# Kernel optimization log

Measured on AMD Instinct MI355X. Metric: run time of the kernel, lower is better.

## Reference

```python
import jax, jax.numpy as jnp
import numpy as np

N_NODES = 50000
N_EDGES = 800000
IN_CH = 256
HID = 512
NUM_LAYERS = 3
EPS = 1e-12  # F.normalize eps


def setup_inputs() -> dict:
    key = jax.random.key(0)
    ks = jax.random.split(key, 2 + 3 * NUM_LAYERS)
    x = jax.random.normal(ks[0], (N_NODES, IN_CH), dtype=jnp.float32)
    edge_index = jax.random.randint(ks[1], (2, N_EDGES), 0, N_NODES, dtype=jnp.int64)
    inp = {"x": x, "edge_index": edge_index}
    dims = [(IN_CH, HID)] + [(HID, HID)] * (NUM_LAYERS - 1)
    for i, (din, dout) in enumerate(dims):
        s = 1.0 / np.sqrt(din)
        inp[f"Wl{i}"] = jax.random.normal(ks[2 + 3 * i], (din, dout), dtype=jnp.float32) * s
        inp[f"bl{i}"] = jnp.zeros((dout,), dtype=jnp.float32)
        inp[f"Wr{i}"] = jax.random.normal(ks[3 + 3 * i], (din, dout), dtype=jnp.float32) * s
    return inp


def _sage_conv(x, src, dst, Wl, bl, Wr):
    # aggr='add': out[dst] += x[src], then lin_l(agg) + lin_r(x), L2 normalize rows
    agg = jax.ops.segment_sum(x[src], dst, num_segments=x.shape[0])  # [N, din]
    out = agg @ Wl + bl + x @ Wr  # [N, dout]
    norm = jnp.maximum(jnp.linalg.norm(out, axis=-1, keepdims=True), EPS)
    return out / norm


def reference(x, edge_index, Wl0, bl0, Wr0, Wl1, bl1, Wr1, Wl2, bl2, Wr2):
    src, dst = edge_index[0], edge_index[1]
    feat = x
    params = [(Wl0, bl0, Wr0), (Wl1, bl1, Wr1), (Wl2, bl2, Wr2)]
    for Wl, bl, Wr in params:
        aggre = _sage_conv(feat, src, dst, Wl, bl, Wr)
        # Dropout(p=0.15) is identity in eval mode
        feat = jax.nn.elu(aggre)
    return feat
```

## Files before the change

kernel.cpp:

```cpp
#include <hip/hip_runtime.h>
#include <math.h>

#define N_NODES 50000
#define M_PAD   50048
#define N_EDGES 800000
#define HID 512

typedef short bf16x8 __attribute__((ext_vector_type(8)));
typedef float f32x4  __attribute__((ext_vector_type(4)));
typedef unsigned short u16x4 __attribute__((ext_vector_type(4)));
typedef unsigned short u16x8 __attribute__((ext_vector_type(8)));

__device__ inline float b2f(unsigned short u) {
    union { unsigned int i; float f; } v; v.i = ((unsigned int)u) << 16; return v.f;
}
__device__ inline unsigned short f2b(float f) {
    union { float f; unsigned int i; } v; v.f = f;
    unsigned int r = v.i + 0x7FFFu + ((v.i >> 16) & 1u);
    return (unsigned short)(r >> 16);
}


__global__ void zero_kernel(int* __restrict__ p, int n) {
    int i = blockIdx.x * blockDim.x + threadIdx.x;
    if (i < n) p[i] = 0;
}

__global__ void detect_kernel(const int* __restrict__ e, int* __restrict__ flag) {
    if (blockIdx.x == 0 && threadIdx.x == 0) {
        int is64 = 1;
        for (int i = 0; i < 16; ++i)
            if (e[2 * i + 1] != 0) is64 = 0;
        *flag = is64;
    }
}

__global__ void hist_kernel(const void* __restrict__ eidx, const int* __restrict__ flag,
                            int* __restrict__ counts) {
    int e = blockIdx.x * blockDim.x + threadIdx.x;
    if (e >= N_EDGES) return;
    int is64 = *flag;
    int d;
    if (is64) d = (int)((const long long*)eidx)[N_EDGES + e];
    else      d = ((const int*)eidx)[N_EDGES + e];
    atomicAdd(&counts[d], 1);
}

__global__ __launch_bounds__(1024) void scan_kernel(const int* __restrict__ counts,
                                                    int* __restrict__ offsets) {
    __shared__ int sums[1024];
    int t = threadIdx.x;
    const int CH = (N_NODES + 1023) / 1024;
    int lo = t * CH;
    int hi = min(lo + CH, N_NODES);
    int s = 0;
    for (int i = lo; i < hi; ++i) s += counts[i];
    sums[t] = s;
    __syncthreads();
    for (int off = 1; off < 1024; off <<= 1) {
        int v = 0;
        if (t >= off) v = sums[t - off];
        __syncthreads();
        sums[t] += v;
        __syncthreads();
    }
    int excl = (t == 0) ? 0 : sums[t - 1];
    for (int i = lo; i < hi; ++i) { offsets[i] = excl; excl += counts[i]; }
    if (t == 1023) offsets[N_NODES] = excl;
}

__global__ void fill_kernel(const void* __restrict__ eidx, const int* __restrict__ flag,
                            const int* __restrict__ offsets, int* __restrict__ cursor,
                            int* __restrict__ edge_src) {
    int e = blockIdx.x * blockDim.x + threadIdx.x;
    if (e >= N_EDGES) return;
    int is64 = *flag;
    int s, d;
    if (is64) {
        const long long* p = (const long long*)eidx;
        s = (int)p[e];
        d = (int)p[N_EDGES + e];
    } else {
        const int* p = (const int*)eidx;
        s = p[e];
        d = p[N_EDGES + e];
    }
    int pos = atomicAdd(&cursor[d], 1);
    edge_src[offsets[d] + pos] = s;
}


__global__ __launch_bounds__(256) void xconv_kernel(const float* __restrict__ x,
                                                    unsigned short* __restrict__ cat1) {
    int id = blockIdx.x * 256 + threadIdx.x;
    if (id >= M_PAD * 64) return;
    int row = id >> 6;
    int c = (id & 63) * 4;
    float4 v = make_float4(0.f, 0.f, 0.f, 0.f);
    if (row < N_NODES) v = *(const float4*)(x + (size_t)row * 256 + c);
    ushort4 h;
    h.x = f2b(v.x); h.y = f2b(v.y); h.z = f2b(v.z); h.w = f2b(v.w);
    *(ushort4*)(cat1 + (size_t)row * 512 + 256 + c) = h;
}

__global__ __launch_bounds__(128) void wconv_kernel(const float* __restrict__ W,
                                                    unsigned short* __restrict__ T,
                                                    int K, int ktot, int off) {
    int n = blockIdx.x;
    for (int k = threadIdx.x; k < K; k += 128)
        T[(size_t)n * ktot + off + k] = f2b(W[(size_t)k * HID + n]);
}


template <int EPL>
__global__ __launch_bounds__(256) void aggregate_kernel(const unsigned short* __restrict__ Fh,
                                                        const int* __restrict__ off,
                                                        const int* __restrict__ esrc,
                                                        unsigned short* __restrict__ Ah) {
    const int STRIDE = 2 * EPL * 64;
    const int wid = threadIdx.x >> 6;
    const int lane = threadIdx.x & 63;
    const int node = blockIdx.x * 4 + wid;
    if (node >= N_NODES) return;
    const int beg = off[node], end = off[node + 1];
    const int deg = end - beg;
    const int lb = lane * EPL;
    using VecT = typename std::conditional<EPL == 8, u16x8, u16x4>::type;

    float a0[EPL], a1[EPL], a2[EPL], a3[EPL];
#pragma unroll
    for (int j = 0; j < EPL; ++j) { a0[j] = 0.f; a1[j] = 0.f; a2[j] = 0.f; a3[j] = 0.f; }

    int idxv = 0;

#define ACC(ARR, S)                                                         \
    {                                                                       \
        VecT v_ = *(const VecT*)(Fh + (size_t)(S) * STRIDE + lb);           \
        _Pragma("unroll")                                                   \
        for (int j_ = 0; j_ < EPL; ++j_) ARR[j_] += b2f(v_[j_]);            \
    }

    for (int i = 0; i < deg; i += 4) {
        const int b = i & 63;
        if (b == 0) idxv = (beg + i + lane < end) ? esrc[beg + i + lane] : 0;
        const int s0 = __shfl(idxv, b);
        const int s1 = __shfl(idxv, b + 1);
        const int s2 = __shfl(idxv, b + 2);
        const int s3 = __shfl(idxv, b + 3);
        ACC(a0, s0);
        if (i + 1 < deg) ACC(a1, s1);
        if (i + 2 < deg) ACC(a2, s2);
        if (i + 3 < deg) ACC(a3, s3);
    }
#undef ACC

    unsigned short* op = Ah + (size_t)node * STRIDE + lb;
    VecT h;
#pragma unroll
    for (int j = 0; j < EPL; ++j) h[j] = f2b(a0[j] + a1[j] + a2[j] + a3[j]);
    __builtin_nontemporal_store(h, (VecT*)op);
}


template <int FINAL>
__global__ __launch_bounds__(512, 2) void gemm_mfma_kernel(
    const unsigned short* __restrict__ A, const unsigned short* __restrict__ B,
    const float* __restrict__ bias, float* __restrict__ outF,
    unsigned short* __restrict__ pre, int K) {
    __shared__ unsigned short S[2 * 12288];
    const int T = gridDim.x;
    const int q = T >> 3, r = T & 7;
    const int xcd = blockIdx.x & 7;
    const int n0 = blockIdx.x >> 3;
    const int g = xcd * q + min(xcd, r) + n0;
    const int bm = (g >> 1) * 128;
    const int bn = (g & 1) * 256;

    const int tid = threadIdx.x;
    const int l = tid & 63;
    const int w = tid >> 6;
    const int wr = (w >> 2) * 64;
    const int wc = (w & 3) * 64;

    const int se = (tid >> 2) * 32 + (tid & 3) * 8;
    const unsigned short* gA  = A + (size_t)(bm + (tid >> 2)) * K + (tid & 3) * 8;
    const unsigned short* gB0 = B + (size_t)(bn + (tid >> 2)) * K + (tid & 3) * 8;
    const unsigned short* gB1 = B + (size_t)(bn + 128 + (tid >> 2)) * K + (tid & 3) * 8;

    f32x4 acc[4][4];
#pragma unroll
    for (int m = 0; m < 4; ++m)
#pragma unroll
        for (int nn = 0; nn < 4; ++nn) acc[m][nn] = (f32x4){0.f, 0.f, 0.f, 0.f};

    const int aoff = (wr + (l & 15)) * 32 + (l >> 4) * 8;
    const int woff = 4096 + (wc + (l & 15)) * 32 + (l >> 4) * 8;
    const int ktiles = K >> 5;

    auto STAGE = [&](int buf, int kt) {
        unsigned short* lb = &S[buf * 12288];
        __builtin_amdgcn_global_load_lds(
            (const __attribute__((address_space(1))) void*)(gA + kt * 32),
            (__attribute__((address_space(3))) void*)(lb + se), 16, 0, 0);
        __builtin_amdgcn_global_load_lds(
            (const __attribute__((address_space(1))) void*)(gB0 + kt * 32),
            (__attribute__((address_space(3))) void*)(lb + 4096 + se), 16, 0, 0);
        __builtin_amdgcn_global_load_lds(
            (const __attribute__((address_space(1))) void*)(gB1 + kt * 32),
            (__attribute__((address_space(3))) void*)(lb + 8192 + se), 16, 0, 0);
    };

    STAGE(0, 0);
    __syncthreads();

    for (int kt = 0; kt < ktiles; ++kt) {
        if (kt + 1 < ktiles) STAGE((kt + 1) & 1, kt + 1);
        const int sb = (kt & 1) * 12288;

        bf16x8 af[4], wf[4];
#pragma unroll
        for (int m = 0; m < 4; ++m)
            af[m] = *(const bf16x8*)&S[sb + aoff + m * 512];
#pragma unroll
        for (int nn = 0; nn < 4; ++nn)
            wf[nn] = *(const bf16x8*)&S[sb + woff + nn * 512];
#pragma unroll
        for (int m = 0; m < 4; ++m)
#pragma unroll
            for (int nn = 0; nn < 4; ++nn)
                acc[m][nn] = __builtin_amdgcn_mfma_f32_16x16x32_bf16(af[m], wf[nn], acc[m][nn], 0, 0, 0);
        __syncthreads();
    }

    const int r0 = bm + wr + (l >> 4) * 4;
    const int c0 = bn + wc + (l & 15);
#pragma unroll
    for (int nn = 0; nn < 4; ++nn) {
        const float bv = bias[c0 + nn * 16];
#pragma unroll
        for (int m = 0; m < 4; ++m) {
#pragma unroll
            for (int j = 0; j < 4; ++j) {
                int gr = r0 + m * 16 + j;
                if (gr < N_NODES) {
                    float val = acc[m][nn][j] + bv;
                    if constexpr (FINAL)
                        outF[(size_t)gr * HID + c0 + nn * 16] = val;
                    else
                        pre[(size_t)gr * HID + c0 + nn * 16] = f2b(val);
                }
            }
        }
    }
}


template <int FINAL>
__global__ __launch_bounds__(256) void norm_elu_kernel(const void* __restrict__ inp,
                                                       float* __restrict__ outF,
                                                       unsigned short* __restrict__ Fh) {
    const int wid = threadIdx.x >> 6;
    const int lane = threadIdx.x & 63;
    const int row = blockIdx.x * 4 + wid;
    if (row >= N_NODES) return;
    float r[8];
    if constexpr (FINAL) {
        const float* p = (const float*)inp + (size_t)row * HID + lane * 8;
        float4 v0 = *(const float4*)p;
        float4 v1 = *(const float4*)(p + 4);
        r[0] = v0.x; r[1] = v0.y; r[2] = v0.z; r[3] = v0.w;
        r[4] = v1.x; r[5] = v1.y; r[6] = v1.z; r[7] = v1.w;
    } else {
        const unsigned short* p = (const unsigned short*)inp + (size_t)row * HID + lane * 8;
        u16x8 v = *(const u16x8*)p;
#pragma unroll
        for (int j = 0; j < 8; ++j) r[j] = b2f(v[j]);
    }
    float ss = 0.f;
#pragma unroll
    for (int j = 0; j < 8; ++j) ss += r[j] * r[j];
#pragma unroll
    for (int o = 32; o > 0; o >>= 1) ss += __shfl_xor(ss, o);
    float inv = 1.f / fmaxf(sqrtf(ss), 1e-12f);
#pragma unroll
    for (int j = 0; j < 8; ++j) {
        r[j] *= inv;
        r[j] = r[j] > 0.f ? r[j] : expm1f(r[j]);
    }
    if constexpr (FINAL) {
        float* q = outF + (size_t)row * HID + lane * 8;
        *(float4*)q = make_float4(r[0], r[1], r[2], r[3]);
        *(float4*)(q + 4) = make_float4(r[4], r[5], r[6], r[7]);
    } else {
        unsigned short* q = Fh + (size_t)row * 1024 + lane * 8;
        u16x8 h;
#pragma unroll
        for (int j = 0; j < 8; ++j) h[j] = f2b(r[j]);
        *(u16x8*)q = h;
    }
}


extern "C" void kernel_launch(void* const* d_in, const int* in_sizes, int n_in,
                              void* d_out, int out_size, void* d_ws, size_t ws_size,
                              hipStream_t stream) {
    const float* x    = (const float*)d_in[0];
    const void*  eidx = d_in[1];
    const float* Wl0 = (const float*)d_in[2];
    const float* bl0 = (const float*)d_in[3];
    const float* Wr0 = (const float*)d_in[4];
    const float* Wl1 = (const float*)d_in[5];
    const float* bl1 = (const float*)d_in[6];
    const float* Wr1 = (const float*)d_in[7];
    const float* Wl2 = (const float*)d_in[8];
    const float* bl2 = (const float*)d_in[9];
    const float* Wr2 = (const float*)d_in[10];
    float* outF = (float*)d_out;
    unsigned short* preB = (unsigned short*)d_out;

    char* ws = (char*)d_ws;
    size_t o = 0;
    auto alloc = [&](size_t bytes) { void* p = ws + o; o += (bytes + 255) & ~(size_t)255; return p; };

    unsigned short* Cat1 = (unsigned short*)alloc((size_t)M_PAD * 512 * 2);
    unsigned short* Cat2 = (unsigned short*)alloc((size_t)M_PAD * 1024 * 2);

    unsigned short* Wcat0 = (unsigned short*)alloc(512 * 512 * 2);
    unsigned short* Wcat1 = (unsigned short*)alloc(512 * 1024 * 2);
    unsigned short* Wcat2 = (unsigned short*)alloc(512 * 1024 * 2);

    int* counts   = (int*)alloc((size_t)2 * N_NODES * 4);
    int* cursor   = counts + N_NODES;
    int* offsets  = (int*)alloc((size_t)(N_NODES + 1) * 4);
    int* edge_src = (int*)alloc((size_t)N_EDGES * 4);
    int* flag     = (int*)alloc(256);

    zero_kernel<<<(2 * N_NODES + 255) / 256, 256, 0, stream>>>(counts, 2 * N_NODES);
    detect_kernel<<<1, 64, 0, stream>>>((const int*)eidx, flag);
    hist_kernel<<<(N_EDGES + 255) / 256, 256, 0, stream>>>(eidx, flag, counts);
    scan_kernel<<<1, 1024, 0, stream>>>(counts, offsets);
    fill_kernel<<<(N_EDGES + 255) / 256, 256, 0, stream>>>(eidx, flag, offsets, cursor, edge_src);

    xconv_kernel<<<(M_PAD * 64 + 255) / 256, 256, 0, stream>>>(x, Cat1);
    wconv_kernel<<<512, 128, 0, stream>>>(Wl0, Wcat0, 256, 512, 0);
    wconv_kernel<<<512, 128, 0, stream>>>(Wr0, Wcat0, 256, 512, 256);
    wconv_kernel<<<512, 128, 0, stream>>>(Wl1, Wcat1, 512, 1024, 0);
    wconv_kernel<<<512, 128, 0, stream>>>(Wr1, Wcat1, 512, 1024, 512);
    wconv_kernel<<<512, 128, 0, stream>>>(Wl2, Wcat2, 512, 1024, 0);
    wconv_kernel<<<512, 128, 0, stream>>>(Wr2, Wcat2, 512, 1024, 512);

    const int ggrid = 2 * (M_PAD / 128);
    const int nchunk = (N_NODES + 3) / 4;

    aggregate_kernel<4><<<nchunk, 256, 0, stream>>>(Cat1 + 256, offsets, edge_src, Cat1);
    gemm_mfma_kernel<0><<<ggrid, 512, 0, stream>>>(Cat1, Wcat0, bl0, nullptr, preB, 512);
    norm_elu_kernel<0><<<nchunk, 256, 0, stream>>>(preB, nullptr, Cat2 + 512);

    aggregate_kernel<8><<<nchunk, 256, 0, stream>>>(Cat2 + 512, offsets, edge_src, Cat2);
    gemm_mfma_kernel<0><<<ggrid, 512, 0, stream>>>(Cat2, Wcat1, bl1, nullptr, preB, 1024);
    norm_elu_kernel<0><<<nchunk, 256, 0, stream>>>(preB, nullptr, Cat2 + 512);

    aggregate_kernel<8><<<nchunk, 256, 0, stream>>>(Cat2 + 512, offsets, edge_src, Cat2);
    gemm_mfma_kernel<1><<<ggrid, 512, 0, stream>>>(Cat2, Wcat2, bl2, outF, nullptr, 1024);
    norm_elu_kernel<1><<<nchunk, 256, 0, stream>>>(outF, outF, nullptr);

    (void)in_sizes; (void)n_in; (void)out_size; (void)ws_size;
}
```

Measured before the change: 783.3 us.

## Overlap root GEMM with neighbor aggregation in a combined heterogeneous kernel

The concatenated [agg|x]·[Wl;Wr] GEMM is split in two. The x·Wr half runs in the same launch as the gather aggregation: the first NP blocks do the MFMA GEMM and the rest aggregate 8 nodes each, so compute-bound and memory-bound work can share the GPU. A second GEMM computes agg·Wl and adds the bf16 partial product P in its epilogue. The weight conversions and the zero/detect launches are merged, which cuts launch count. The cost is an extra bf16 round trip of P through memory, extra rounding of the partial product, and a halved K per GEMM.

```diff
diff --git a/kernel.cpp b/kernel.cpp
--- a/kernel.cpp
+++ b/kernel.cpp
@@ -21,16 +21,14 @@
 }
 
 
-__global__ void zero_kernel(int* __restrict__ p, int n) {
+__global__ void zero_detect_kernel(int* __restrict__ p, int n,
+                                   const int* __restrict__ e, int* __restrict__ flag) {
     int i = blockIdx.x * blockDim.x + threadIdx.x;
     if (i < n) p[i] = 0;
-}
-
-__global__ void detect_kernel(const int* __restrict__ e, int* __restrict__ flag) {
     if (blockIdx.x == 0 && threadIdx.x == 0) {
         int is64 = 1;
-        for (int i = 0; i < 16; ++i)
-            if (e[2 * i + 1] != 0) is64 = 0;
+        for (int k = 0; k < 16; ++k)
+            if (e[2 * k + 1] != 0) is64 = 0;
         *flag = is64;
     }
 }
@@ -91,7 +89,7 @@
 
 
 __global__ __launch_bounds__(256) void xconv_kernel(const float* __restrict__ x,
-                                                    unsigned short* __restrict__ cat1) {
+                                                    unsigned short* __restrict__ feat) {
     int id = blockIdx.x * 256 + threadIdx.x;
     if (id >= M_PAD * 64) return;
     int row = id >> 6;
@@ -100,73 +98,162 @@
     if (row < N_NODES) v = *(const float4*)(x + (size_t)row * 256 + c);
     ushort4 h;
     h.x = f2b(v.x); h.y = f2b(v.y); h.z = f2b(v.z); h.w = f2b(v.w);
-    *(ushort4*)(cat1 + (size_t)row * 512 + 256 + c) = h;
-}
-
-__global__ __launch_bounds__(128) void wconv_kernel(const float* __restrict__ W,
-                                                    unsigned short* __restrict__ T,
-                                                    int K, int ktot, int off) {
+    *(ushort4*)(feat + (size_t)row * 256 + c) = h;
+}
+
+__global__ __launch_bounds__(128) void wconv_all_kernel(
+    const float* __restrict__ Wl0, const float* __restrict__ Wr0,
+    const float* __restrict__ Wl1, const float* __restrict__ Wr1,
+    const float* __restrict__ Wl2, const float* __restrict__ Wr2,
+    unsigned short* __restrict__ Tl0, unsigned short* __restrict__ Tr0,
+    unsigned short* __restrict__ Tl1, unsigned short* __restrict__ Tr1,
+    unsigned short* __restrict__ Tl2, unsigned short* __restrict__ Tr2) {
+    const int y = blockIdx.y;
+    const float* W = (y == 0) ? Wl0 : (y == 1) ? Wr0 : (y == 2) ? Wl1
+                   : (y == 3) ? Wr1 : (y == 4) ? Wl2 : Wr2;
+    unsigned short* T = (y == 0) ? Tl0 : (y == 1) ? Tr0 : (y == 2) ? Tl1
+                      : (y == 3) ? Tr1 : (y == 4) ? Tl2 : Tr2;
+    const int K = (y < 2) ? 256 : 512;
     int n = blockIdx.x;
     for (int k = threadIdx.x; k < K; k += 128)
-        T[(size_t)n * ktot + off + k] = f2b(W[(size_t)k * HID + n]);
-}
-
-
-template <int EPL>
-__global__ __launch_bounds__(256) void aggregate_kernel(const unsigned short* __restrict__ Fh,
-                                                        const int* __restrict__ off,
-                                                        const int* __restrict__ esrc,
-                                                        unsigned short* __restrict__ Ah) {
-    const int STRIDE = 2 * EPL * 64;
-    const int wid = threadIdx.x >> 6;
-    const int lane = threadIdx.x & 63;
-    const int node = blockIdx.x * 4 + wid;
-    if (node >= N_NODES) return;
-    const int beg = off[node], end = off[node + 1];
-    const int deg = end - beg;
-    const int lb = lane * EPL;
-    using VecT = typename std::conditional<EPL == 8, u16x8, u16x4>::type;
-
-    float a0[EPL], a1[EPL], a2[EPL], a3[EPL];
-#pragma unroll
-    for (int j = 0; j < EPL; ++j) { a0[j] = 0.f; a1[j] = 0.f; a2[j] = 0.f; a3[j] = 0.f; }
-
-    int idxv = 0;
-
-#define ACC(ARR, S)                                                         \
-    {                                                                       \
-        VecT v_ = *(const VecT*)(Fh + (size_t)(S) * STRIDE + lb);           \
-        _Pragma("unroll")                                                   \
-        for (int j_ = 0; j_ < EPL; ++j_) ARR[j_] += b2f(v_[j_]);            \
-    }
-
-    for (int i = 0; i < deg; i += 4) {
-        const int b = i & 63;
-        if (b == 0) idxv = (beg + i + lane < end) ? esrc[beg + i + lane] : 0;
-        const int s0 = __shfl(idxv, b);
-        const int s1 = __shfl(idxv, b + 1);
-        const int s2 = __shfl(idxv, b + 2);
-        const int s3 = __shfl(idxv, b + 3);
-        ACC(a0, s0);
-        if (i + 1 < deg) ACC(a1, s1);
-        if (i + 2 < deg) ACC(a2, s2);
-        if (i + 3 < deg) ACC(a3, s3);
-    }
+        T[(size_t)n * K + k] = f2b(W[(size_t)k * HID + n]);
+}
+
+
+template <int DIN>
+__global__ __launch_bounds__(512, 2) void fat_kernel(
+    const unsigned short* __restrict__ feat, const unsigned short* __restrict__ W2t,
+    unsigned short* __restrict__ P,
+    const int* __restrict__ off, const int* __restrict__ esrc,
+    unsigned short* __restrict__ agg, int NP) {
+    __shared__ unsigned short S[2 * 12288];
+    const int tid = threadIdx.x;
+
+    if ((int)blockIdx.x < NP) {
+        const int T = NP;
+        const int q = T >> 3, r = T & 7;
+        const int xcd = blockIdx.x & 7;
+        const int n0 = blockIdx.x >> 3;
+        const int g = xcd * q + min(xcd, r) + n0;
+        const int bm = (g >> 1) * 128;
+        const int bn = (g & 1) * 256;
+
+        const int l = tid & 63;
+        const int w = tid >> 6;
+        const int wr = (w >> 2) * 64;
+        const int wc = (w & 3) * 64;
+
+        const int se = (tid >> 2) * 32 + (tid & 3) * 8;
+        const unsigned short* gA  = feat + (size_t)(bm + (tid >> 2)) * DIN + (tid & 3) * 8;
+        const unsigned short* gB0 = W2t + (size_t)(bn + (tid >> 2)) * DIN + (tid & 3) * 8;
+        const unsigned short* gB1 = W2t + (size_t)(bn + 128 + (tid >> 2)) * DIN + (tid & 3) * 8;
+
+        f32x4 acc[4][4];
+#pragma unroll
+        for (int m = 0; m < 4; ++m)
+#pragma unroll
+            for (int nn = 0; nn < 4; ++nn) acc[m][nn] = (f32x4){0.f, 0.f, 0.f, 0.f};
+
+        const int aoff = (wr + (l & 15)) * 32 + (l >> 4) * 8;
+        const int woff = 4096 + (wc + (l & 15)) * 32 + (l >> 4) * 8;
+        const int ktiles = DIN >> 5;
+
+        auto STAGE = [&](int buf, int kt) {
+            unsigned short* lb = &S[buf * 12288];
+            __builtin_amdgcn_global_load_lds(
+                (const __attribute__((address_space(1))) void*)(gA + kt * 32),
+                (__attribute__((address_space(3))) void*)(lb + se), 16, 0, 0);
+            __builtin_amdgcn_global_load_lds(
+                (const __attribute__((address_space(1))) void*)(gB0 + kt * 32),
+                (__attribute__((address_space(3))) void*)(lb + 4096 + se), 16, 0, 0);
+            __builtin_amdgcn_global_load_lds(
+                (const __attribute__((address_space(1))) void*)(gB1 + kt * 32),
+                (__attribute__((address_space(3))) void*)(lb + 8192 + se), 16, 0, 0);
+        };
+
+        STAGE(0, 0);
+        __syncthreads();
+        for (int kt = 0; kt < ktiles; ++kt) {
+            if (kt + 1 < ktiles) STAGE((kt + 1) & 1, kt + 1);
+            const int sb = (kt & 1) * 12288;
+            bf16x8 af[4], wf[4];
+#pragma unroll
+            for (int m = 0; m < 4; ++m)
+                af[m] = *(const bf16x8*)&S[sb + aoff + m * 512];
+#pragma unroll
+            for (int nn = 0; nn < 4; ++nn)
+                wf[nn] = *(const bf16x8*)&S[sb + woff + nn * 512];
+#pragma unroll
+            for (int m = 0; m < 4; ++m)
+#pragma unroll
+                for (int nn = 0; nn < 4; ++nn)
+                    acc[m][nn] = __builtin_amdgcn_mfma_f32_16x16x32_bf16(af[m], wf[nn], acc[m][nn], 0, 0, 0);
+            __syncthreads();
+        }
+
+        const int r0 = bm + wr + (l >> 4) * 4;
+        const int c0 = bn + wc + (l & 15);
+#pragma unroll
+        for (int nn = 0; nn < 4; ++nn) {
+#pragma unroll
+            for (int m = 0; m < 4; ++m) {
+#pragma unroll
+                for (int j = 0; j < 4; ++j) {
+                    int gr = r0 + m * 16 + j;
+                    if (gr < N_NODES)
+                        P[(size_t)gr * HID + c0 + nn * 16] = f2b(acc[m][nn][j]);
+                }
+            }
+        }
+    } else {
+        const int EPL = DIN / 64;
+        const int wid = tid >> 6;
+        const int lane = tid & 63;
+        const int node = (blockIdx.x - NP) * 8 + wid;
+        if (node >= N_NODES) return;
+        const int beg = off[node], end = off[node + 1];
+        const int deg = end - beg;
+        const int lb = lane * EPL;
+        using VecT = typename std::conditional<EPL == 8, u16x8, u16x4>::type;
+
+        float a0[EPL], a1[EPL], a2[EPL], a3[EPL];
+#pragma unroll
+        for (int j = 0; j < EPL; ++j) { a0[j] = 0.f; a1[j] = 0.f; a2[j] = 0.f; a3[j] = 0.f; }
+
+        int idxv = 0;
+#define ACC(ARR, SS)                                                        \
+        {                                                                   \
+            VecT v_ = *(const VecT*)(feat + (size_t)(SS) * DIN + lb);       \
+            _Pragma("unroll")                                               \
+            for (int j_ = 0; j_ < EPL; ++j_) ARR[j_] += b2f(v_[j_]);        \
+        }
+        for (int i = 0; i < deg; i += 4) {
+            const int b = i & 63;
+            if (b == 0) idxv = (beg + i + lane < end) ? esrc[beg + i + lane] : 0;
+            const int s0 = __shfl(idxv, b);
+            const int s1 = __shfl(idxv, b + 1);
+            const int s2 = __shfl(idxv, b + 2);
+            const int s3 = __shfl(idxv, b + 3);
+            ACC(a0, s0);
+            if (i + 1 < deg) ACC(a1, s1);
+            if (i + 2 < deg) ACC(a2, s2);
+            if (i + 3 < deg) ACC(a3, s3);
+        }
 #undef ACC
-
-    unsigned short* op = Ah + (size_t)node * STRIDE + lb;
-    VecT h;
-#pragma unroll
-    for (int j = 0; j < EPL; ++j) h[j] = f2b(a0[j] + a1[j] + a2[j] + a3[j]);
-    __builtin_nontemporal_store(h, (VecT*)op);
-}
-
-
-template <int FINAL>
-__global__ __launch_bounds__(512, 2) void gemm_mfma_kernel(
+        unsigned short* op = agg + (size_t)node * DIN + lb;
+        VecT h;
+#pragma unroll
+        for (int j = 0; j < EPL; ++j) h[j] = f2b(a0[j] + a1[j] + a2[j] + a3[j]);
+        __builtin_nontemporal_store(h, (VecT*)op);
+    }
+}
+
+
+template <int FINAL, int DIN>
+__global__ __launch_bounds__(512, 2) void gemm2_kernel(
     const unsigned short* __restrict__ A, const unsigned short* __restrict__ B,
-    const float* __restrict__ bias, float* __restrict__ outF,
-    unsigned short* __restrict__ pre, int K) {
+    const unsigned short* __restrict__ P, const float* __restrict__ bias,
+    float* __restrict__ outF, unsigned short* __restrict__ pre) {
     __shared__ unsigned short S[2 * 12288];
     const int T = gridDim.x;
     const int q = T >> 3, r = T & 7;
@@ -183,9 +270,9 @@
     const int wc = (w & 3) * 64;
 
     const int se = (tid >> 2) * 32 + (tid & 3) * 8;
-    const unsigned short* gA  = A + (size_t)(bm + (tid >> 2)) * K + (tid & 3) * 8;
-    const unsigned short* gB0 = B + (size_t)(bn + (tid >> 2)) * K + (tid & 3) * 8;
-    const unsigned short* gB1 = B + (size_t)(bn + 128 + (tid >> 2)) * K + (tid & 3) * 8;
+    const unsigned short* gA  = A + (size_t)(bm + (tid >> 2)) * DIN + (tid & 3) * 8;
+    const unsigned short* gB0 = B + (size_t)(bn + (tid >> 2)) * DIN + (tid & 3) * 8;
+    const unsigned short* gB1 = B + (size_t)(bn + 128 + (tid >> 2)) * DIN + (tid & 3) * 8;
 
     f32x4 acc[4][4];
 #pragma unroll
@@ -195,7 +282,7 @@
 
     const int aoff = (wr + (l & 15)) * 32 + (l >> 4) * 8;
     const int woff = 4096 + (wc + (l & 15)) * 32 + (l >> 4) * 8;
-    const int ktiles = K >> 5;
+    const int ktiles = DIN >> 5;
 
     auto STAGE = [&](int buf, int kt) {
         unsigned short* lb = &S[buf * 12288];
@@ -212,11 +299,9 @@
 
     STAGE(0, 0);
     __syncthreads();
-
     for (int kt = 0; kt < ktiles; ++kt) {
         if (kt + 1 < ktiles) STAGE((kt + 1) & 1, kt + 1);
         const int sb = (kt & 1) * 12288;
-
         bf16x8 af[4], wf[4];
 #pragma unroll
         for (int m = 0; m < 4; ++m)
@@ -243,7 +328,8 @@
             for (int j = 0; j < 4; ++j) {
                 int gr = r0 + m * 16 + j;
                 if (gr < N_NODES) {
-                    float val = acc[m][nn][j] + bv;
+                    float val = acc[m][nn][j] + bv
+                              + b2f(P[(size_t)gr * HID + c0 + nn * 16]);
                     if constexpr (FINAL)
                         outF[(size_t)gr * HID + c0 + nn * 16] = val;
                     else
@@ -258,7 +344,7 @@
 template <int FINAL>
 __global__ __launch_bounds__(256) void norm_elu_kernel(const void* __restrict__ inp,
                                                        float* __restrict__ outF,
-                                                       unsigned short* __restrict__ Fh) {
+                                                       unsigned short* __restrict__ feat) {
     const int wid = threadIdx.x >> 6;
     const int lane = threadIdx.x & 63;
     const int row = blockIdx.x * 4 + wid;
@@ -288,15 +374,15 @@
         r[j] = r[j] > 0.f ? r[j] : expm1f(r[j]);
     }
     if constexpr (FINAL) {
-        float* q = outF + (size_t)row * HID + lane * 8;
-        *(float4*)q = make_float4(r[0], r[1], r[2], r[3]);
-        *(float4*)(q + 4) = make_float4(r[4], r[5], r[6], r[7]);
+        float* qp = outF + (size_t)row * HID + lane * 8;
+        *(float4*)qp = make_float4(r[0], r[1], r[2], r[3]);
+        *(float4*)(qp + 4) = make_float4(r[4], r[5], r[6], r[7]);
     } else {
-        unsigned short* q = Fh + (size_t)row * 1024 + lane * 8;
+        unsigned short* qp = feat + (size_t)row * HID + lane * 8;
         u16x8 h;
 #pragma unroll
         for (int j = 0; j < 8; ++j) h[j] = f2b(r[j]);
-        *(u16x8*)q = h;
+        *(u16x8*)qp = h;
     }
 }
 
@@ -322,12 +408,16 @@
     size_t o = 0;
     auto alloc = [&](size_t bytes) { void* p = ws + o; o += (bytes + 255) & ~(size_t)255; return p; };
 
-    unsigned short* Cat1 = (unsigned short*)alloc((size_t)M_PAD * 512 * 2);
-    unsigned short* Cat2 = (unsigned short*)alloc((size_t)M_PAD * 1024 * 2);
-
-    unsigned short* Wcat0 = (unsigned short*)alloc(512 * 512 * 2);
-    unsigned short* Wcat1 = (unsigned short*)alloc(512 * 1024 * 2);
-    unsigned short* Wcat2 = (unsigned short*)alloc(512 * 1024 * 2);
+    unsigned short* featB = (unsigned short*)alloc((size_t)M_PAD * 512 * 2);
+    unsigned short* aggB  = (unsigned short*)alloc((size_t)M_PAD * 512 * 2);
+    unsigned short* Pbuf  = (unsigned short*)alloc((size_t)M_PAD * 512 * 2);
+
+    unsigned short* Wl0t = (unsigned short*)alloc(512 * 256 * 2);
+    unsigned short* Wr0t = (unsigned short*)alloc(512 * 256 * 2);
+    unsigned short* Wl1t = (unsigned short*)alloc(512 * 512 * 2);
+    unsigned short* Wr1t = (unsigned short*)alloc(512 * 512 * 2);
+    unsigned short* Wl2t = (unsigned short*)alloc(512 * 512 * 2);
+    unsigned short* Wr2t = (unsigned short*)alloc(512 * 512 * 2);
 
     int* counts   = (int*)alloc((size_t)2 * N_NODES * 4);
     int* cursor   = counts + N_NODES;
@@ -335,33 +425,33 @@
     int* edge_src = (int*)alloc((size_t)N_EDGES * 4);
     int* flag     = (int*)alloc(256);
 
-    zero_kernel<<<(2 * N_NODES + 255) / 256, 256, 0, stream>>>(counts, 2 * N_NODES);
-    detect_kernel<<<1, 64, 0, stream>>>((const int*)eidx, flag);
+    zero_detect_kernel<<<(2 * N_NODES + 255) / 256, 256, 0, stream>>>(
+        counts, 2 * N_NODES, (const int*)eidx, flag);
     hist_kernel<<<(N_EDGES + 255) / 256, 256, 0, stream>>>(eidx, flag, counts);
     scan_kernel<<<1, 1024, 0, stream>>>(counts, offsets);
     fill_kernel<<<(N_EDGES + 255) / 256, 256, 0, stream>>>(eidx, flag, offsets, cursor, edge_src);
 
-    xconv_kernel<<<(M_PAD * 64 + 255) / 256, 256, 0, stream>>>(x, Cat1);
-    wconv_kernel<<<512, 128, 0, stream>>>(Wl0, Wcat0, 256, 512, 0);
-    wconv_kernel<<<512, 128, 0, stream>>>(Wr0, Wcat0, 256, 512, 256);
-    wconv_kernel<<<512, 128, 0, stream>>>(Wl1, Wcat1, 512, 1024, 0);
-    wconv_kernel<<<512, 128, 0, stream>>>(Wr1, Wcat1, 512, 1024, 512);
-    wconv_kernel<<<512, 128, 0, stream>>>(Wl2, Wcat2, 512, 1024, 0);
-    wconv_kernel<<<512, 128, 0, stream>>>(Wr2, Wcat2, 512, 1024, 512);
-
-    const int ggrid = 2 * (M_PAD / 128);
+    xconv_kernel<<<(M_PAD * 64 + 255) / 256, 256, 0, stream>>>(x, featB);
+    {
+        dim3 wgrid(512, 6);
+        wconv_all_kernel<<<wgrid, 128, 0, stream>>>(Wl0, Wr0, Wl1, Wr1, Wl2, Wr2,
+                                                    Wl0t, Wr0t, Wl1t, Wr1t, Wl2t, Wr2t);
+    }
+
+    const int NP = 2 * (M_PAD / 128);
+    const int NG = (N_NODES + 7) / 8;
     const int nchunk = (N_NODES + 3) / 4;
 
-    aggregate_kernel<4><<<nchunk, 256, 0, stream>>>(Cat1 + 256, offsets, edge_src, Cat1);
-    gemm_mfma_kernel<0><<<ggrid, 512, 0, stream>>>(Cat1, Wcat0, bl0, nullptr, preB, 512);
-    norm_elu_kernel<0><<<nchunk, 256, 0, stream>>>(preB, nullptr, Cat2 + 512);
-
-    aggregate_kernel<8><<<nchunk, 256, 0, stream>>>(Cat2 + 512, offsets, edge_src, Cat2);
-    gemm_mfma_kernel<0><<<ggrid, 512, 0, stream>>>(Cat2, Wcat1, bl1, nullptr, preB, 1024);
-    norm_elu_kernel<0><<<nchunk, 256, 0, stream>>>(preB, nullptr, Cat2 + 512);
-
-    aggregate_kernel<8><<<nchunk, 256, 0, stream>>>(Cat2 + 512, offsets, edge_src, Cat2);
-    gemm_mfma_kernel<1><<<ggrid, 512, 0, stream>>>(Cat2, Wcat2, bl2, outF, nullptr, 1024);
+    fat_kernel<256><<<NP + NG, 512, 0, stream>>>(featB, Wr0t, Pbuf, offsets, edge_src, aggB, NP);
+    gemm2_kernel<0, 256><<<NP, 512, 0, stream>>>(aggB, Wl0t, Pbuf, bl0, nullptr, preB);
+    norm_elu_kernel<0><<<nchunk, 256, 0, stream>>>(preB, nullptr, featB);
+
+    fat_kernel<512><<<NP + NG, 512, 0, stream>>>(featB, Wr1t, Pbuf, offsets, edge_src, aggB, NP);
+    gemm2_kernel<0, 512><<<NP, 512, 0, stream>>>(aggB, Wl1t, Pbuf, bl1, nullptr, preB);
+    norm_elu_kernel<0><<<nchunk, 256, 0, stream>>>(preB, nullptr, featB);
+
+    fat_kernel<512><<<NP + NG, 512, 0, stream>>>(featB, Wr2t, Pbuf, offsets, edge_src, aggB, NP);
+    gemm2_kernel<1, 512><<<NP, 512, 0, stream>>>(aggB, Wl2t, Pbuf, bl2, outF, nullptr);
     norm_elu_kernel<1><<<nchunk, 256, 0, stream>>>(outF, outF, nullptr);
 
     (void)in_sizes; (void)n_in; (void)out_size; (void)ws_size;
```

After: 1.084 ms. +38.3%, slower.

## Replace GEMM with 256x256-tile, 8-phase pipelined MFMA kernel with swizzled LDS

Applied to the files above, without the earlier changes.

Swaps the 128x256-tile double-buffered GEMM for a 256x256-tile kernel with BK=64. Each K-tile is split into half-tile phases that interleave global-to-LDS staging with MFMA work, using explicit vmcnt waits, barriers and s_setprio. It adds an XOR swizzle to the LDS layout to cut bank conflicts and pads M to a multiple of 256. The aim is more operand reuse per LDS load and better overlap of memory traffic with compute, at the cost of one block per CU (128KB LDS, more registers). The zero and detect setup kernels are also merged into one launch.

```diff
diff --git a/kernel.cpp b/kernel.cpp
--- a/kernel.cpp
+++ b/kernel.cpp
@@ -2,7 +2,7 @@
 #include <math.h>
 
 #define N_NODES 50000
-#define M_PAD   50048
+#define M_PAD   50176
 #define N_EDGES 800000
 #define HID 512
 
@@ -21,16 +21,14 @@
 }
 
 
-__global__ void zero_kernel(int* __restrict__ p, int n) {
+__global__ void zero_detect_kernel(int* __restrict__ p, int n,
+                                   const int* __restrict__ e, int* __restrict__ flag) {
     int i = blockIdx.x * blockDim.x + threadIdx.x;
     if (i < n) p[i] = 0;
-}
-
-__global__ void detect_kernel(const int* __restrict__ e, int* __restrict__ flag) {
     if (blockIdx.x == 0 && threadIdx.x == 0) {
         int is64 = 1;
-        for (int i = 0; i < 16; ++i)
-            if (e[2 * i + 1] != 0) is64 = 0;
+        for (int k = 0; k < 16; ++k)
+            if (e[2 * k + 1] != 0) is64 = 0;
         *flag = is64;
     }
 }
@@ -132,14 +130,12 @@
     for (int j = 0; j < EPL; ++j) { a0[j] = 0.f; a1[j] = 0.f; a2[j] = 0.f; a3[j] = 0.f; }
 
     int idxv = 0;
-
 #define ACC(ARR, S)                                                         \
     {                                                                       \
         VecT v_ = *(const VecT*)(Fh + (size_t)(S) * STRIDE + lb);           \
         _Pragma("unroll")                                                   \
         for (int j_ = 0; j_ < EPL; ++j_) ARR[j_] += b2f(v_[j_]);            \
     }
-
     for (int i = 0; i < deg; i += 4) {
         const int b = i & 63;
         if (b == 0) idxv = (beg + i + lane < end) ? esrc[beg + i + lane] : 0;
@@ -153,7 +149,6 @@
         if (i + 3 < deg) ACC(a3, s3);
     }
 #undef ACC
-
     unsigned short* op = Ah + (size_t)node * STRIDE + lb;
     VecT h;
 #pragma unroll
@@ -163,91 +158,116 @@
 
 
 template <int FINAL>
-__global__ __launch_bounds__(512, 2) void gemm_mfma_kernel(
+__global__ __launch_bounds__(512, 1) void gemm8_kernel(
     const unsigned short* __restrict__ A, const unsigned short* __restrict__ B,
     const float* __restrict__ bias, float* __restrict__ outF,
     unsigned short* __restrict__ pre, int K) {
-    __shared__ unsigned short S[2 * 12288];
-    const int T = gridDim.x;
-    const int q = T >> 3, r = T & 7;
-    const int xcd = blockIdx.x & 7;
-    const int n0 = blockIdx.x >> 3;
-    const int g = xcd * q + min(xcd, r) + n0;
-    const int bm = (g >> 1) * 128;
-    const int bn = (g & 1) * 256;
-
+    __shared__ unsigned short S[65536];
     const int tid = threadIdx.x;
     const int l = tid & 63;
     const int w = tid >> 6;
-    const int wr = (w >> 2) * 64;
-    const int wc = (w & 3) * 64;
-
-    const int se = (tid >> 2) * 32 + (tid & 3) * 8;
-    const unsigned short* gA  = A + (size_t)(bm + (tid >> 2)) * K + (tid & 3) * 8;
-    const unsigned short* gB0 = B + (size_t)(bn + (tid >> 2)) * K + (tid & 3) * 8;
-    const unsigned short* gB1 = B + (size_t)(bn + 128 + (tid >> 2)) * K + (tid & 3) * 8;
-
-    f32x4 acc[4][4];
-#pragma unroll
-    for (int m = 0; m < 4; ++m)
-#pragma unroll
-        for (int nn = 0; nn < 4; ++nn) acc[m][nn] = (f32x4){0.f, 0.f, 0.f, 0.f};
-
-    const int aoff = (wr + (l & 15)) * 32 + (l >> 4) * 8;
-    const int woff = 4096 + (wc + (l & 15)) * 32 + (l >> 4) * 8;
-    const int ktiles = K >> 5;
-
-    auto STAGE = [&](int buf, int kt) {
-        unsigned short* lb = &S[buf * 12288];
+    const int wm = w >> 2;
+    const int wn = w & 3;
+    const int li = l & 15;
+    const int ch = l >> 4;
+
+    const int g = (blockIdx.x & 7) * 49 + (blockIdx.x >> 3);
+    const int bm = (g >> 1) * 256;
+    const int bn = (g & 1) * 256;
+
+    const int cswz = (ch ^ ((li >> 1) & 3)) * 8;
+    const int srow = tid >> 2;
+    const int scol = (((tid & 3) ^ ((tid >> 3) & 3)) * 8);
+
+    const int ktiles = K >> 6;
+    const int nit = ktiles >> 1;
+
+    auto STAGE = [&](int t, int r) {
+        const bool isA = (r & 1) == 0;
+        const int kh = r >> 1;
+        const unsigned short* gsrc = isA ? (A + (size_t)(bm + srow) * K)
+                                         : (B + (size_t)(bn + srow) * K);
+        const unsigned short* g0 = gsrc + t * 64 + kh * 32 + scol;
+        const unsigned short* g1 = g0 + (size_t)128 * K;
+        unsigned short* lds = S + (t & 1) * 32768 + (isA ? 0 : 16384) + kh * 8192 + tid * 8;
         __builtin_amdgcn_global_load_lds(
-            (const __attribute__((address_space(1))) void*)(gA + kt * 32),
-            (__attribute__((address_space(3))) void*)(lb + se), 16, 0, 0);
+            (const __attribute__((address_space(1))) void*)g0,
+            (__attribute__((address_space(3))) void*)lds, 16, 0, 0);
         __builtin_amdgcn_global_load_lds(
-            (const __attribute__((address_space(1))) void*)(gB0 + kt * 32),
-            (__attribute__((address_space(3))) void*)(lb + 4096 + se), 16, 0, 0);
-        __builtin_amdgcn_global_load_lds(
-            (const __attribute__((address_space(1))) void*)(gB1 + kt * 32),
-            (__attribute__((address_space(3))) void*)(lb + 8192 + se), 16, 0, 0);
+            (const __attribute__((address_space(1))) void*)g1,
+            (__attribute__((address_space(3))) void*)(lds + 4096), 16, 0, 0);
     };
 
-    STAGE(0, 0);
-    __syncthreads();
-
-    for (int kt = 0; kt < ktiles; ++kt) {
-        if (kt + 1 < ktiles) STAGE((kt + 1) & 1, kt + 1);
-        const int sb = (kt & 1) * 12288;
-
-        bf16x8 af[4], wf[4];
-#pragma unroll
-        for (int m = 0; m < 4; ++m)
-            af[m] = *(const bf16x8*)&S[sb + aoff + m * 512];
-#pragma unroll
-        for (int nn = 0; nn < 4; ++nn)
-            wf[nn] = *(const bf16x8*)&S[sb + woff + nn * 512];
-#pragma unroll
-        for (int m = 0; m < 4; ++m)
-#pragma unroll
-            for (int nn = 0; nn < 4; ++nn)
-                acc[m][nn] = __builtin_amdgcn_mfma_f32_16x16x32_bf16(af[m], wf[nn], acc[m][nn], 0, 0, 0);
-        __syncthreads();
-    }
-
-    const int r0 = bm + wr + (l >> 4) * 4;
-    const int c0 = bn + wc + (l & 15);
-#pragma unroll
-    for (int nn = 0; nn < 4; ++nn) {
-        const float bv = bias[c0 + nn * 16];
-#pragma unroll
-        for (int m = 0; m < 4; ++m) {
+    f32x4 acc[8][4];
+#pragma unroll
+    for (int m = 0; m < 8; ++m)
+#pragma unroll
+        for (int n = 0; n < 4; ++n) acc[m][n] = (f32x4){0.f, 0.f, 0.f, 0.f};
+
+    bf16x8 bfrag[4];
+
+    STAGE(0, 0); STAGE(0, 1); STAGE(0, 2); STAGE(0, 3);
+    STAGE(1, 0); STAGE(1, 1);
+    asm volatile("s_waitcnt vmcnt(4)" ::: "memory");
+    __builtin_amdgcn_s_barrier();
+
+#define PHASE(VM, TCUR, KK, FRH, STT, STR)                                      \
+    {                                                                           \
+        const int sb = ((TCUR) & 1) * 32768;                                    \
+        bf16x8 af[4];                                                           \
+        _Pragma("unroll")                                                       \
+        for (int fr = 0; fr < 4; ++fr)                                          \
+            af[fr] = *(const bf16x8*)&S[sb + (KK)*8192 +                        \
+                (wm * 128 + ((FRH)*4 + fr) * 16 + li) * 32 + cswz];             \
+        if ((FRH) == 0) {                                                       \
+            _Pragma("unroll")                                                   \
+            for (int fc = 0; fc < 4; ++fc)                                      \
+                bfrag[fc] = *(const bf16x8*)&S[sb + 16384 + (KK)*8192 +         \
+                    (wn * 64 + fc * 16 + li) * 32 + cswz];                      \
+        }                                                                       \
+        STAGE(((STT) < ktiles) ? (STT) : (STT) - 2, (STR));                     \
+        if (VM) asm volatile("s_waitcnt vmcnt(4)" ::: "memory");                \
+        __builtin_amdgcn_s_barrier();                                           \
+        __builtin_amdgcn_s_setprio(1);                                          \
+        _Pragma("unroll")                                                       \
+        for (int fr = 0; fr < 4; ++fr)                                          \
+            _Pragma("unroll")                                                   \
+            for (int fc = 0; fc < 4; ++fc)                                      \
+                acc[(FRH)*4 + fr][fc] = __builtin_amdgcn_mfma_f32_16x16x32_bf16(\
+                    af[fr], bfrag[fc], acc[(FRH)*4 + fr][fc], 0, 0, 0);         \
+        __builtin_amdgcn_s_setprio(0);                                          \
+        __builtin_amdgcn_s_barrier();                                           \
+    }
+
+    for (int i = 0; i < nit; ++i) {
+        const int t0 = 2 * i;
+        PHASE(0, t0,     0, 0, t0 + 1, 2);
+        PHASE(0, t0,     0, 1, t0 + 1, 3);
+        PHASE(0, t0,     1, 0, t0 + 2, 0);
+        PHASE(1, t0,     1, 1, t0 + 2, 1);
+        PHASE(0, t0 + 1, 0, 0, t0 + 2, 2);
+        PHASE(0, t0 + 1, 0, 1, t0 + 2, 3);
+        PHASE(0, t0 + 1, 1, 0, t0 + 3, 0);
+        PHASE(1, t0 + 1, 1, 1, t0 + 3, 1);
+    }
+#undef PHASE
+
+    const int r0 = bm + wm * 128 + ch * 4;
+    const int c0 = bn + wn * 64 + li;
+#pragma unroll
+    for (int fc = 0; fc < 4; ++fc) {
+        const float bv = bias[c0 + fc * 16];
+#pragma unroll
+        for (int fr = 0; fr < 8; ++fr) {
 #pragma unroll
             for (int j = 0; j < 4; ++j) {
-                int gr = r0 + m * 16 + j;
+                int gr = r0 + fr * 16 + j;
                 if (gr < N_NODES) {
-                    float val = acc[m][nn][j] + bv;
+                    float val = acc[fr][fc][j] + bv;
                     if constexpr (FINAL)
-                        outF[(size_t)gr * HID + c0 + nn * 16] = val;
+                        outF[(size_t)gr * HID + c0 + fc * 16] = val;
                     else
-                        pre[(size_t)gr * HID + c0 + nn * 16] = f2b(val);
+                        pre[(size_t)gr * HID + c0 + fc * 16] = f2b(val);
                 }
             }
         }
@@ -335,8 +355,8 @@
     int* edge_src = (int*)alloc((size_t)N_EDGES * 4);
     int* flag     = (int*)alloc(256);
 
-    zero_kernel<<<(2 * N_NODES + 255) / 256, 256, 0, stream>>>(counts, 2 * N_NODES);
-    detect_kernel<<<1, 64, 0, stream>>>((const int*)eidx, flag);
+    zero_detect_kernel<<<(2 * N_NODES + 255) / 256, 256, 0, stream>>>(
+        counts, 2 * N_NODES, (const int*)eidx, flag);
     hist_kernel<<<(N_EDGES + 255) / 256, 256, 0, stream>>>(eidx, flag, counts);
     scan_kernel<<<1, 1024, 0, stream>>>(counts, offsets);
     fill_kernel<<<(N_EDGES + 255) / 256, 256, 0, stream>>>(eidx, flag, offsets, cursor, edge_src);
@@ -349,19 +369,19 @@
     wconv_kernel<<<512, 128, 0, stream>>>(Wl2, Wcat2, 512, 1024, 0);
     wconv_kernel<<<512, 128, 0, stream>>>(Wr2, Wcat2, 512, 1024, 512);
 
-    const int ggrid = 2 * (M_PAD / 128);
+    const int ggrid = 2 * (M_PAD / 256);
     const int nchunk = (N_NODES + 3) / 4;
 
     aggregate_kernel<4><<<nchunk, 256, 0, stream>>>(Cat1 + 256, offsets, edge_src, Cat1);
-    gemm_mfma_kernel<0><<<ggrid, 512, 0, stream>>>(Cat1, Wcat0, bl0, nullptr, preB, 512);
+    gemm8_kernel<0><<<ggrid, 512, 0, stream>>>(Cat1, Wcat0, bl0, nullptr, preB, 512);
     norm_elu_kernel<0><<<nchunk, 256, 0, stream>>>(preB, nullptr, Cat2 + 512);
 
     aggregate_kernel<8><<<nchunk, 256, 0, stream>>>(Cat2 + 512, offsets, edge_src, Cat2);
-    gemm_mfma_kernel<0><<<ggrid, 512, 0, stream>>>(Cat2, Wcat1, bl1, nullptr, preB, 1024);
+    gemm8_kernel<0><<<ggrid, 512, 0, stream>>>(Cat2, Wcat1, bl1, nullptr, preB, 1024);
     norm_elu_kernel<0><<<nchunk, 256, 0, stream>>>(preB, nullptr, Cat2 + 512);
 
     aggregate_kernel<8><<<nchunk, 256, 0, stream>>>(Cat2 + 512, offsets, edge_src, Cat2);
-    gemm_mfma_kernel<1><<<ggrid, 512, 0, stream>>>(Cat2, Wcat2, bl2, outF, nullptr, 1024);
+    gemm8_kernel<1><<<ggrid, 512, 0, stream>>>(Cat2, Wcat2, bl2, outF, nullptr, 1024);
     norm_elu_kernel<1><<<nchunk, 256, 0, stream>>>(outF, outF, nullptr);
 
     (void)in_sizes; (void)n_in; (void)out_size; (void)ws_size;
```

New measurement: 801.9 us. 1.02x slower.
